# Performance work log

Measured on AMD Instinct MI355X. Metric: run time of the kernel, lower is better.

The kernel has to match this reference:

```python
import jax, jax.numpy as jnp
import numpy as np
import math

N_NODES = 100000
N_EDGES = 3200000
NFEAT = 512
NHID = 256
NCLASS = 16
NLAYERS = 8
LAMDA = 0.5
ALPHA = 0.1


def setup_inputs() -> dict:
    key = jax.random.key(0)
    ks = jax.random.split(key, 10)
    x = jax.random.normal(ks[0], (N_NODES, NFEAT), dtype=jnp.float32)
    edge_src = jax.random.randint(ks[1], (N_EDGES,), 0, N_NODES, dtype=jnp.int32)
    edge_dst = jax.random.randint(ks[2], (N_EDGES,), 0, N_NODES, dtype=jnp.int32)
    edge_w = jax.random.uniform(ks[3], (N_EDGES,), dtype=jnp.float32)
    # fcs[0]: Linear(nfeat, nhidden); fcs[1]: Linear(nhidden, nclass)
    s0 = 1.0 / math.sqrt(NFEAT)
    w0 = jax.random.uniform(ks[4], (NFEAT, NHID), minval=-s0, maxval=s0, dtype=jnp.float32)
    b0 = jax.random.uniform(ks[5], (NHID,), minval=-s0, maxval=s0, dtype=jnp.float32)
    # conv weights: uniform(-1/sqrt(out_features), +), out_features = nhidden
    sc = 1.0 / math.sqrt(NHID)
    conv_w = jax.random.uniform(ks[6], (NLAYERS, NHID, NHID), minval=-sc, maxval=sc, dtype=jnp.float32)
    w1 = jax.random.uniform(ks[7], (NHID, NCLASS), minval=-sc, maxval=sc, dtype=jnp.float32)
    b1 = jax.random.uniform(ks[8], (NCLASS,), minval=-sc, maxval=sc, dtype=jnp.float32)
    return {"x": x, "edge_src": edge_src, "edge_dst": edge_dst, "edge_w": edge_w,
            "w0": w0, "b0": b0, "conv_w": conv_w, "w1": w1, "b1": b1}


def _spmm(edge_src, edge_dst, edge_w, h):
    # torch.spmm(adj, h): out[i] = sum_j adj[i,j] * h[j], adj in COO (dst=row, src=col)
    msgs = edge_w[:, None] * h[edge_src]            # [E, H] irregular gather
    return jax.ops.segment_sum(msgs, edge_dst, num_segments=h.shape[0])


def reference(x, edge_src, edge_dst, edge_w, w0, b0, conv_w, w1, b1):
    # eval mode: F.dropout is identity
    h = jax.nn.relu(x @ w0 + b0)                    # [N, NHID]
    h0 = h
    for i in range(NLAYERS):
        theta = math.log(LAMDA / (i + 1) + 1.0)
        hi = _spmm(edge_src, edge_dst, edge_w, h)   # sparse aggregate
        support = (1.0 - ALPHA) * hi + ALPHA * h0   # initial residual (GCNII)
        out = theta * (support @ conv_w[i]) + (1.0 - theta) * support
        h = jax.nn.relu(out + h)                    # layer residual
    return jax.nn.sigmoid(h @ w1 + b1)              # [N, NCLASS]
```

## Files before the change

kernel.cpp:

```cpp
#include <hip/hip_runtime.h>
#include <math.h>

#define N_NODES 100000
#define N_EDGES 3200000
#define NFEAT 512
#define NHID 256
#define NCLASS 16
#define NLAYERS 8

#define SCAN_CHUNK 1024
#define NB ((N_NODES + SCAN_CHUNK - 1) / SCAN_CHUNK)

typedef float f32x4 __attribute__((ext_vector_type(4)));
typedef short s16x8 __attribute__((ext_vector_type(8)));

__device__ __forceinline__ unsigned short bf16_rne(float f) {
  unsigned u = __float_as_uint(f);
  unsigned r = 0x7fffu + ((u >> 16) & 1u);
  return (unsigned short)((u + r) >> 16);
}
__device__ __forceinline__ float bf16_tof(unsigned short h) {
  return __uint_as_float(((unsigned)h) << 16);
}

__global__ void k_hist(const int* __restrict__ dst, int* __restrict__ cnt) {
  int i = blockIdx.x * 256 + threadIdx.x;
  if (i < N_EDGES) atomicAdd(&cnt[dst[i]], 1);
}

__global__ void k_blocksum(const int* __restrict__ cnt, int* __restrict__ bs) {
  __shared__ int red[256];
  int b = blockIdx.x, t = threadIdx.x;
  int s = 0;
  int base = b * SCAN_CHUNK;
  for (int j = 0; j < 4; ++j) {
    int i = base + t + j * 256;
    if (i < N_NODES) s += cnt[i];
  }
  red[t] = s;
  __syncthreads();
  for (int off = 128; off > 0; off >>= 1) {
    if (t < off) red[t] += red[t + off];
    __syncthreads();
  }
  if (t == 0) bs[b] = red[0];
}

__global__ void k_scan_top(int* __restrict__ bs, int* __restrict__ rp) {
  if (threadIdx.x == 0) {
    int run = 0;
    for (int b = 0; b < NB; ++b) { int v = bs[b]; bs[b] = run; run += v; }
    rp[N_NODES] = run;
  }
}

__global__ void k_scan_write(const int* __restrict__ cnt, const int* __restrict__ bs,
                             int* __restrict__ rp) {
  __shared__ int tot[256];
  int b = blockIdx.x, t = threadIdx.x;
  int base = b * SCAN_CHUNK + t * 4;
  int v0 = 0, v1 = 0, v2 = 0, v3 = 0;
  if (base + 0 < N_NODES) v0 = cnt[base + 0];
  if (base + 1 < N_NODES) v1 = cnt[base + 1];
  if (base + 2 < N_NODES) v2 = cnt[base + 2];
  if (base + 3 < N_NODES) v3 = cnt[base + 3];
  int tsum = v0 + v1 + v2 + v3;
  tot[t] = tsum;
  __syncthreads();
  for (int off = 1; off < 256; off <<= 1) {
    int v = 0;
    if (t >= off) v = tot[t - off];
    __syncthreads();
    if (t >= off) tot[t] += v;
    __syncthreads();
  }
  int excl = tot[t] - tsum + bs[b];
  if (base + 0 < N_NODES) rp[base + 0] = excl;
  if (base + 1 < N_NODES) rp[base + 1] = excl + v0;
  if (base + 2 < N_NODES) rp[base + 2] = excl + v0 + v1;
  if (base + 3 < N_NODES) rp[base + 3] = excl + v0 + v1 + v2;
}

__global__ void k_fill(const int* __restrict__ src, const int* __restrict__ dst,
                       const float* __restrict__ w, const int* __restrict__ rp,
                       int* __restrict__ fill, int* __restrict__ col,
                       float* __restrict__ val) {
  int i = blockIdx.x * 256 + threadIdx.x;
  if (i < N_EDGES) {
    int d = dst[i];
    int pos = rp[d] + atomicAdd(&fill[d], 1);
    col[pos] = src[i];
    val[pos] = w[i];
  }
}

__global__ __launch_bounds__(256)
void k_spmm_half(const int* __restrict__ rp, const int* __restrict__ col,
                 const float* __restrict__ val, const float* __restrict__ h,
                 const float* __restrict__ h0, float* __restrict__ sup, int f0) {
  int wave = threadIdx.x >> 6;
  int lane = threadIdx.x & 63;
  int node = blockIdx.x * 4 + wave;
  if (node >= N_NODES) return;
  int e0 = rp[node], e1 = rp[node + 1];
  const float2* __restrict__ hv = (const float2*)h;
  int fo = (f0 >> 1) + lane;

  float2 a0 = make_float2(0.f, 0.f);
  float2 a1 = make_float2(0.f, 0.f);
  float2 a2 = make_float2(0.f, 0.f);
  float2 a3 = make_float2(0.f, 0.f);

  int e = e0;
  for (; e + 4 <= e1; e += 4) {
    int s0 = col[e], s1 = col[e + 1], s2 = col[e + 2], s3 = col[e + 3];
    float w0 = val[e], w1 = val[e + 1], w2 = val[e + 2], w3 = val[e + 3];
    float2 v0 = hv[(size_t)s0 * 128 + fo];
    float2 v1 = hv[(size_t)s1 * 128 + fo];
    float2 v2 = hv[(size_t)s2 * 128 + fo];
    float2 v3 = hv[(size_t)s3 * 128 + fo];
    a0.x += w0 * v0.x; a0.y += w0 * v0.y;
    a1.x += w1 * v1.x; a1.y += w1 * v1.y;
    a2.x += w2 * v2.x; a2.y += w2 * v2.y;
    a3.x += w3 * v3.x; a3.y += w3 * v3.y;
  }
  for (; e < e1; ++e) {
    int s0 = col[e];
    float w0 = val[e];
    float2 v0 = hv[(size_t)s0 * 128 + fo];
    a0.x += w0 * v0.x; a0.y += w0 * v0.y;
  }

  float2 acc;
  acc.x = (a0.x + a1.x) + (a2.x + a3.x);
  acc.y = (a0.y + a1.y) + (a2.y + a3.y);

  float2 z = ((const float2*)h0)[(size_t)node * 128 + fo];
  float2 o;
  o.x = 0.9f * acc.x + 0.1f * z.x;
  o.y = 0.9f * acc.y + 0.1f * z.y;
  ((float2*)sup)[(size_t)node * 128 + fo] = o;
}

__global__ void k_splitw(const float* __restrict__ W, unsigned short* __restrict__ hi,
                         unsigned short* __restrict__ lo, int K) {
  int mat = blockIdx.y;
  const float* Wm = W + (size_t)mat * K * NHID;
  unsigned short* hm = hi + (size_t)mat * K * NHID;
  unsigned short* lm = lo + (size_t)mat * K * NHID;
  int idx = blockIdx.x * 256 + threadIdx.x;
  if (idx >= K * NHID) return;
  int k = idx >> 8;
  int n = idx & 255;
  float f = Wm[idx];
  unsigned short h = bf16_rne(f);
  unsigned short l = bf16_rne(f - bf16_tof(h));
  hm[(size_t)n * K + k] = h;
  lm[(size_t)n * K + k] = l;
}

#define PADK 40

template <int MODE>
__global__ __launch_bounds__(256)
void k_gemm_mfma(const float* __restrict__ A, const unsigned short* __restrict__ Bh_g,
                 const unsigned short* __restrict__ Bl_g, int K,
                 const float* __restrict__ bias, const float* __restrict__ hin,
                 float* __restrict__ out1, float* __restrict__ out2, float theta) {
  __shared__ unsigned short Ah[128][PADK];
  __shared__ unsigned short Al[128][PADK];
  __shared__ unsigned short Bh[128][PADK];
  __shared__ unsigned short Bl[128][PADK];
  const int bm = blockIdx.x * 128, bn = blockIdx.y * 128;
  const int tid = threadIdx.x;
  const int lane = tid & 63, wave = tid >> 6;
  const int wr = (wave >> 1) * 64;
  const int wc = (wave & 1) * 64;
  const int l16 = lane & 15, lk = lane >> 4;

  f32x4 acc[4][4];
#pragma unroll
  for (int i = 0; i < 4; ++i)
#pragma unroll
    for (int j = 0; j < 4; ++j)
#pragma unroll
      for (int q = 0; q < 4; ++q) acc[i][j][q] = 0.f;

  const int srow = tid >> 3;
  const int skq = (tid & 7) * 4;

  for (int kc = 0; kc < K; kc += 32) {
#pragma unroll
    for (int it = 0; it < 4; ++it) {
      int row = srow + it * 32;
      int gm = bm + row;
      float4 f = make_float4(0.f, 0.f, 0.f, 0.f);
      if (gm < N_NODES) f = *(const float4*)&A[(size_t)gm * K + kc + skq];
      unsigned short h0 = bf16_rne(f.x), h1 = bf16_rne(f.y);
      unsigned short h2 = bf16_rne(f.z), h3 = bf16_rne(f.w);
      ushort4 hv = make_ushort4(h0, h1, h2, h3);
      ushort4 lv = make_ushort4(bf16_rne(f.x - bf16_tof(h0)),
                                bf16_rne(f.y - bf16_tof(h1)),
                                bf16_rne(f.z - bf16_tof(h2)),
                                bf16_rne(f.w - bf16_tof(h3)));
      *(ushort4*)&Ah[row][skq] = hv;
      *(ushort4*)&Al[row][skq] = lv;
    }
#pragma unroll
    for (int it = 0; it < 4; ++it) {
      int row = srow + it * 32;
      size_t go = (size_t)(bn + row) * K + kc + skq;
      *(ushort4*)&Bh[row][skq] = *(const ushort4*)&Bh_g[go];
      *(ushort4*)&Bl[row][skq] = *(const ushort4*)&Bl_g[go];
    }
    __syncthreads();

    s16x8 ah[4], al[4], bh[4], bl[4];
#pragma unroll
    for (int i = 0; i < 4; ++i) {
      ah[i] = *(const s16x8*)&Ah[wr + i * 16 + l16][lk * 8];
      al[i] = *(const s16x8*)&Al[wr + i * 16 + l16][lk * 8];
      bh[i] = *(const s16x8*)&Bh[wc + i * 16 + l16][lk * 8];
      bl[i] = *(const s16x8*)&Bl[wc + i * 16 + l16][lk * 8];
    }
#pragma unroll
    for (int i = 0; i < 4; ++i)
#pragma unroll
      for (int j = 0; j < 4; ++j)
        acc[i][j] = __builtin_amdgcn_mfma_f32_16x16x32_bf16(ah[i], bh[j], acc[i][j], 0, 0, 0);
#pragma unroll
    for (int i = 0; i < 4; ++i)
#pragma unroll
      for (int j = 0; j < 4; ++j)
        acc[i][j] = __builtin_amdgcn_mfma_f32_16x16x32_bf16(ah[i], bl[j], acc[i][j], 0, 0, 0);
#pragma unroll
    for (int i = 0; i < 4; ++i)
#pragma unroll
      for (int j = 0; j < 4; ++j)
        acc[i][j] = __builtin_amdgcn_mfma_f32_16x16x32_bf16(al[i], bh[j], acc[i][j], 0, 0, 0);
    __syncthreads();
  }

  const float omt = 1.f - theta;
#pragma unroll
  for (int i = 0; i < 4; ++i) {
#pragma unroll
    for (int j = 0; j < 4; ++j) {
      int gn = bn + wc + j * 16 + l16;
#pragma unroll
      for (int q = 0; q < 4; ++q) {
        int gm = bm + wr + i * 16 + lk * 4 + q;
        if (gm >= N_NODES) continue;
        size_t r = (size_t)gm * NHID + gn;
        float v = acc[i][j][q];
        if (MODE == 0) {
          float o = fmaxf(v + bias[gn], 0.f);
          out1[r] = o;
          out2[r] = o;
        } else {
          float s = A[r];
          float o = fmaxf(theta * v + omt * s + hin[r], 0.f);
          out1[r] = o;
        }
      }
    }
  }
}

__global__ __launch_bounds__(256)
void k_final(const float* __restrict__ h, const float* __restrict__ w1,
             const float* __restrict__ b1, float* __restrict__ out) {
  __shared__ float ws[NHID * NCLASS];
  int t = threadIdx.x;
  for (int i = t; i < NHID * NCLASS; i += 256) ws[i] = w1[i];
  __syncthreads();
  int node = blockIdx.x * 16 + (t >> 4);
  int c = t & 15;
  if (node >= N_NODES) return;
  float acc = b1[c];
  const float* hr = &h[(size_t)node * NHID];
  for (int k = 0; k < NHID; k += 4) {
    float4 hv = *(const float4*)&hr[k];
    acc += hv.x * ws[(k + 0) * NCLASS + c];
    acc += hv.y * ws[(k + 1) * NCLASS + c];
    acc += hv.z * ws[(k + 2) * NCLASS + c];
    acc += hv.w * ws[(k + 3) * NCLASS + c];
  }
  out[(size_t)node * NCLASS + c] = 1.f / (1.f + __expf(-acc));
}

extern "C" void kernel_launch(void* const* d_in, const int* in_sizes, int n_in,
                              void* d_out, int out_size, void* d_ws, size_t ws_size,
                              hipStream_t stream) {
  const float* x        = (const float*)d_in[0];
  const int*   edge_src = (const int*)d_in[1];
  const int*   edge_dst = (const int*)d_in[2];
  const float* edge_w   = (const float*)d_in[3];
  const float* w0       = (const float*)d_in[4];
  const float* b0       = (const float*)d_in[5];
  const float* conv_w   = (const float*)d_in[6];
  const float* w1       = (const float*)d_in[7];
  const float* b1       = (const float*)d_in[8];
  float* out = (float*)d_out;

  char* ws = (char*)d_ws;
  size_t off = 0;
  auto alloc = [&](size_t bytes) {
    size_t o = off;
    off = (off + bytes + 255) & ~(size_t)255;
    return (void*)(ws + o);
  };
  float* h   = (float*)alloc((size_t)N_NODES * NHID * 4);
  float* h0  = (float*)alloc((size_t)N_NODES * NHID * 4);
  float* sup = (float*)alloc((size_t)N_NODES * NHID * 4);
  int*   rp  = (int*)alloc((size_t)(N_NODES + 1) * 4);
  int*   cnt = (int*)alloc((size_t)N_NODES * 4);
  int*   col = (int*)alloc((size_t)N_EDGES * 4);
  float* val = (float*)alloc((size_t)N_EDGES * 4);
  int*   bs  = (int*)alloc((size_t)NB * 4);
  unsigned short* w0t_hi = (unsigned short*)alloc((size_t)NFEAT * NHID * 2);
  unsigned short* w0t_lo = (unsigned short*)alloc((size_t)NFEAT * NHID * 2);
  unsigned short* cwt_hi = (unsigned short*)alloc((size_t)NLAYERS * NHID * NHID * 2);
  unsigned short* cwt_lo = (unsigned short*)alloc((size_t)NLAYERS * NHID * NHID * 2);
  (void)ws_size;

  (void)hipMemsetAsync(cnt, 0, (size_t)N_NODES * 4, stream);
  k_hist<<<(N_EDGES + 255) / 256, 256, 0, stream>>>(edge_dst, cnt);
  k_blocksum<<<NB, 256, 0, stream>>>(cnt, bs);
  k_scan_top<<<1, 64, 0, stream>>>(bs, rp);
  k_scan_write<<<NB, 256, 0, stream>>>(cnt, bs, rp);
  (void)hipMemsetAsync(cnt, 0, (size_t)N_NODES * 4, stream);
  k_fill<<<(N_EDGES + 255) / 256, 256, 0, stream>>>(edge_src, edge_dst, edge_w, rp,
                                                    cnt, col, val);

  k_splitw<<<dim3((NFEAT * NHID + 255) / 256, 1), 256, 0, stream>>>(w0, w0t_hi, w0t_lo, NFEAT);
  k_splitw<<<dim3((NHID * NHID + 255) / 256, NLAYERS), 256, 0, stream>>>(conv_w, cwt_hi, cwt_lo, NHID);

  dim3 g0((N_NODES + 127) / 128, NHID / 128);
  k_gemm_mfma<0><<<g0, 256, 0, stream>>>(x, w0t_hi, w0t_lo, NFEAT, b0, nullptr, h, h0, 0.f);

  for (int i = 0; i < NLAYERS; ++i) {
    float theta = logf(0.5f / (float)(i + 1) + 1.0f);
    k_spmm_half<<<(N_NODES + 3) / 4, 256, 0, stream>>>(rp, col, val, h, h0, sup, 0);
    k_spmm_half<<<(N_NODES + 3) / 4, 256, 0, stream>>>(rp, col, val, h, h0, sup, 128);
    const unsigned short* whi = cwt_hi + (size_t)i * NHID * NHID;
    const unsigned short* wlo = cwt_lo + (size_t)i * NHID * NHID;
    k_gemm_mfma<1><<<g0, 256, 0, stream>>>(sup, whi, wlo, NHID, nullptr, h, h, nullptr, theta);
  }

  k_final<<<(N_NODES + 15) / 16, 256, 0, stream>>>(h, w1, b1, out);
}
```

Measured before the change: 5.855 ms.

## Pre-split SpMM output to bf16 hi/lo and double-buffer full-width MFMA GEMM

The SpMM now writes its support output already split into bf16 hi/lo halves, so the layer GEMM no longer converts fp32 A tiles itself. The GEMM becomes a 512-thread kernel covering all 256 output columns per block, so A is read once instead of once per column half. It streams A and B into double-buffered LDS via async global-to-LDS loads, overlapping loads with MFMA. The epilogue stages results through LDS for coalesced float4 stores. This adds a large LDS footprint (96KB) that limits occupancy, and the residual term is rebuilt from the hi+lo pair instead of read as fp32.

```diff
diff --git a/kernel.cpp b/kernel.cpp
--- a/kernel.cpp
+++ b/kernel.cpp
@@ -21,6 +21,12 @@
 }
 __device__ __forceinline__ float bf16_tof(unsigned short h) {
   return __uint_as_float(((unsigned)h) << 16);
+}
+
+__device__ __forceinline__ void async16(void* lds_dst, const void* gsrc) {
+  __builtin_amdgcn_global_load_lds(
+      (const __attribute__((address_space(1))) unsigned int*)gsrc,
+      (__attribute__((address_space(3))) unsigned int*)lds_dst, 16, 0, 0);
 }
 
 __global__ void k_hist(const int* __restrict__ dst, int* __restrict__ cnt) {
@@ -97,7 +103,9 @@
 __global__ __launch_bounds__(256)
 void k_spmm_half(const int* __restrict__ rp, const int* __restrict__ col,
                  const float* __restrict__ val, const float* __restrict__ h,
-                 const float* __restrict__ h0, float* __restrict__ sup, int f0) {
+                 const float* __restrict__ h0,
+                 unsigned short* __restrict__ sup_hi,
+                 unsigned short* __restrict__ sup_lo, int f0) {
   int wave = threadIdx.x >> 6;
   int lane = threadIdx.x & 63;
   int node = blockIdx.x * 4 + wave;
@@ -136,10 +144,13 @@
   acc.y = (a0.y + a1.y) + (a2.y + a3.y);
 
   float2 z = ((const float2*)h0)[(size_t)node * 128 + fo];
-  float2 o;
-  o.x = 0.9f * acc.x + 0.1f * z.x;
-  o.y = 0.9f * acc.y + 0.1f * z.y;
-  ((float2*)sup)[(size_t)node * 128 + fo] = o;
+  float ox = 0.9f * acc.x + 0.1f * z.x;
+  float oy = 0.9f * acc.y + 0.1f * z.y;
+  unsigned short hx = bf16_rne(ox), hy = bf16_rne(oy);
+  unsigned short lx = bf16_rne(ox - bf16_tof(hx));
+  unsigned short ly = bf16_rne(oy - bf16_tof(hy));
+  ((ushort2*)sup_hi)[(size_t)node * 128 + fo] = make_ushort2(hx, hy);
+  ((ushort2*)sup_lo)[(size_t)node * 128 + fo] = make_ushort2(lx, ly);
 }
 
 __global__ void k_splitw(const float* __restrict__ W, unsigned short* __restrict__ hi,
@@ -159,24 +170,21 @@
   lm[(size_t)n * K + k] = l;
 }
 
-#define PADK 40
-
 template <int MODE>
-__global__ __launch_bounds__(256)
-void k_gemm_mfma(const float* __restrict__ A, const unsigned short* __restrict__ Bh_g,
-                 const unsigned short* __restrict__ Bl_g, int K,
-                 const float* __restrict__ bias, const float* __restrict__ hin,
-                 float* __restrict__ out1, float* __restrict__ out2, float theta) {
-  __shared__ unsigned short Ah[128][PADK];
-  __shared__ unsigned short Al[128][PADK];
-  __shared__ unsigned short Bh[128][PADK];
-  __shared__ unsigned short Bl[128][PADK];
-  const int bm = blockIdx.x * 128, bn = blockIdx.y * 128;
+__global__ __launch_bounds__(512)
+void k_gemm2(const float* __restrict__ Af,
+             const unsigned short* __restrict__ Ah_g,
+             const unsigned short* __restrict__ Al_g,
+             const unsigned short* __restrict__ Bh_g,
+             const unsigned short* __restrict__ Bl_g, int K,
+             const float* __restrict__ bias, const float* __restrict__ hin,
+             float* __restrict__ out1, float* __restrict__ out2, float theta) {
+  __shared__ unsigned short pool[49152];
   const int tid = threadIdx.x;
-  const int lane = tid & 63, wave = tid >> 6;
-  const int wr = (wave >> 1) * 64;
-  const int wc = (wave & 1) * 64;
+  const int lane = tid & 63, w = tid >> 6;
+  const int wr = w >> 2, wc = w & 3;
   const int l16 = lane & 15, lk = lane >> 4;
+  const int bm = blockIdx.x * 128;
 
   f32x4 acc[4][4];
 #pragma unroll
@@ -186,42 +194,74 @@
 #pragma unroll
       for (int q = 0; q < 4; ++q) acc[i][j][q] = 0.f;
 
-  const int srow = tid >> 3;
-  const int skq = (tid & 7) * 4;
-
-  for (int kc = 0; kc < K; kc += 32) {
-#pragma unroll
-    for (int it = 0; it < 4; ++it) {
-      int row = srow + it * 32;
-      int gm = bm + row;
-      float4 f = make_float4(0.f, 0.f, 0.f, 0.f);
-      if (gm < N_NODES) f = *(const float4*)&A[(size_t)gm * K + kc + skq];
-      unsigned short h0 = bf16_rne(f.x), h1 = bf16_rne(f.y);
-      unsigned short h2 = bf16_rne(f.z), h3 = bf16_rne(f.w);
+  auto stageB = [&](int buf, int kc) {
+#pragma unroll
+    for (int u = 0; u < 2; ++u) {
+      int fb = w * 2 + u;
+      size_t go = (size_t)(fb * 16 + l16) * K + kc + lk * 8;
+      async16(&pool[16384 + buf * 8192 + fb * 512], &Bh_g[go]);
+      async16(&pool[32768 + buf * 8192 + fb * 512], &Bl_g[go]);
+    }
+  };
+  auto stageA1 = [&](int buf, int kc) {
+    size_t go = (size_t)(bm + w * 16 + l16) * K + kc + lk * 8;
+    async16(&pool[0 + buf * 4096 + w * 512], &Ah_g[go]);
+    async16(&pool[8192 + buf * 4096 + w * 512], &Al_g[go]);
+  };
+  float4 fa0, fa1;
+  auto stageA0_issue = [&](int kc) {
+    int m0 = tid >> 3, k00 = (tid & 7) * 4;
+    int m1 = (tid + 512) >> 3, k01 = ((tid + 512) & 7) * 4;
+    fa0 = make_float4(0.f, 0.f, 0.f, 0.f);
+    fa1 = fa0;
+    if (bm + m0 < N_NODES) fa0 = *(const float4*)&Af[(size_t)(bm + m0) * K + kc + k00];
+    if (bm + m1 < N_NODES) fa1 = *(const float4*)&Af[(size_t)(bm + m1) * K + kc + k01];
+  };
+  auto stageA0_write = [&](int buf) {
+#pragma unroll
+    for (int p = 0; p < 2; ++p) {
+      int f = tid + p * 512;
+      int m = f >> 3, k0 = (f & 7) * 4;
+      float4 fv = p ? fa1 : fa0;
+      int L = (m >> 4) * 64 + (m & 15) + (k0 >> 3) * 16;
+      unsigned short h0 = bf16_rne(fv.x), h1 = bf16_rne(fv.y);
+      unsigned short h2 = bf16_rne(fv.z), h3 = bf16_rne(fv.w);
       ushort4 hv = make_ushort4(h0, h1, h2, h3);
-      ushort4 lv = make_ushort4(bf16_rne(f.x - bf16_tof(h0)),
-                                bf16_rne(f.y - bf16_tof(h1)),
-                                bf16_rne(f.z - bf16_tof(h2)),
-                                bf16_rne(f.w - bf16_tof(h3)));
-      *(ushort4*)&Ah[row][skq] = hv;
-      *(ushort4*)&Al[row][skq] = lv;
-    }
-#pragma unroll
-    for (int it = 0; it < 4; ++it) {
-      int row = srow + it * 32;
-      size_t go = (size_t)(bn + row) * K + kc + skq;
-      *(ushort4*)&Bh[row][skq] = *(const ushort4*)&Bh_g[go];
-      *(ushort4*)&Bl[row][skq] = *(const ushort4*)&Bl_g[go];
-    }
-    __syncthreads();
-
+      ushort4 lv = make_ushort4(bf16_rne(fv.x - bf16_tof(h0)),
+                                bf16_rne(fv.y - bf16_tof(h1)),
+                                bf16_rne(fv.z - bf16_tof(h2)),
+                                bf16_rne(fv.w - bf16_tof(h3)));
+      *(ushort4*)&pool[0 + buf * 4096 + L * 8 + (k0 & 7)] = hv;
+      *(ushort4*)&pool[8192 + buf * 4096 + L * 8 + (k0 & 7)] = lv;
+    }
+  };
+
+  if (MODE == 0) { stageA0_issue(0); stageA0_write(0); }
+  else stageA1(0, 0);
+  stageB(0, 0);
+  __syncthreads();
+
+  const int nt = K / 32;
+  int buf = 0;
+  for (int t = 0; t < nt; ++t) {
+    const bool pf = (t + 1 < nt);
+    if (pf) {
+      if (MODE == 0) stageA0_issue((t + 1) * 32);
+      else stageA1(buf ^ 1, (t + 1) * 32);
+      stageB(buf ^ 1, (t + 1) * 32);
+    }
     s16x8 ah[4], al[4], bh[4], bl[4];
 #pragma unroll
     for (int i = 0; i < 4; ++i) {
-      ah[i] = *(const s16x8*)&Ah[wr + i * 16 + l16][lk * 8];
-      al[i] = *(const s16x8*)&Al[wr + i * 16 + l16][lk * 8];
-      bh[i] = *(const s16x8*)&Bh[wc + i * 16 + l16][lk * 8];
-      bl[i] = *(const s16x8*)&Bl[wc + i * 16 + l16][lk * 8];
+      int fb = wr * 4 + i;
+      ah[i] = *(const s16x8*)&pool[0 + buf * 4096 + fb * 512 + lane * 8];
+      al[i] = *(const s16x8*)&pool[8192 + buf * 4096 + fb * 512 + lane * 8];
+    }
+#pragma unroll
+    for (int j = 0; j < 4; ++j) {
+      int fb = wc * 4 + j;
+      bh[j] = *(const s16x8*)&pool[16384 + buf * 8192 + fb * 512 + lane * 8];
+      bl[j] = *(const s16x8*)&pool[32768 + buf * 8192 + fb * 512 + lane * 8];
     }
 #pragma unroll
     for (int i = 0; i < 4; ++i)
@@ -238,32 +278,64 @@
 #pragma unroll
       for (int j = 0; j < 4; ++j)
         acc[i][j] = __builtin_amdgcn_mfma_f32_16x16x32_bf16(al[i], bh[j], acc[i][j], 0, 0, 0);
-    __syncthreads();
-  }
-
+    if (MODE == 0 && pf) stageA0_write(buf ^ 1);
+    __syncthreads();
+    buf ^= 1;
+  }
+
+  float* Cst = (float*)pool;
   const float omt = 1.f - theta;
-#pragma unroll
-  for (int i = 0; i < 4; ++i) {
-#pragma unroll
-    for (int j = 0; j < 4; ++j) {
-      int gn = bn + wc + j * 16 + l16;
-#pragma unroll
-      for (int q = 0; q < 4; ++q) {
-        int gm = bm + wr + i * 16 + lk * 4 + q;
-        if (gm >= N_NODES) continue;
-        size_t r = (size_t)gm * NHID + gn;
-        float v = acc[i][j][q];
-        if (MODE == 0) {
-          float o = fmaxf(v + bias[gn], 0.f);
-          out1[r] = o;
-          out2[r] = o;
-        } else {
-          float s = A[r];
-          float o = fmaxf(theta * v + omt * s + hin[r], 0.f);
-          out1[r] = o;
+  for (int g = 0; g < 4; ++g) {
+    if (wr == (g >> 1)) {
+#pragma unroll
+      for (int ii = 0; ii < 2; ++ii) {
+        int i = (g & 1) * 2 + ii;
+#pragma unroll
+        for (int j = 0; j < 4; ++j) {
+          int colc = wc * 64 + j * 16 + l16;
+#pragma unroll
+          for (int q = 0; q < 4; ++q) {
+            int lr = ii * 16 + lk * 4 + q;
+            Cst[lr * 260 + colc] = acc[i][j][q];
+          }
         }
       }
     }
+    __syncthreads();
+#pragma unroll
+    for (int p = 0; p < 4; ++p) {
+      int f = tid + p * 512;
+      int row = f >> 6, c4 = (f & 63) * 4;
+      int gm = bm + g * 32 + row;
+      if (gm < N_NODES) {
+        float4 v = *(const float4*)&Cst[row * 260 + c4];
+        size_t r = (size_t)gm * NHID + c4;
+        float4 o;
+        if (MODE == 0) {
+          float4 bb = *(const float4*)&bias[c4];
+          o.x = fmaxf(v.x + bb.x, 0.f);
+          o.y = fmaxf(v.y + bb.y, 0.f);
+          o.z = fmaxf(v.z + bb.z, 0.f);
+          o.w = fmaxf(v.w + bb.w, 0.f);
+          *(float4*)&out1[r] = o;
+          *(float4*)&out2[r] = o;
+        } else {
+          ushort4 sh = *(const ushort4*)&Ah_g[r];
+          ushort4 sl = *(const ushort4*)&Al_g[r];
+          float4 hv = *(const float4*)&hin[r];
+          float sx = bf16_tof(sh.x) + bf16_tof(sl.x);
+          float sy = bf16_tof(sh.y) + bf16_tof(sl.y);
+          float sz = bf16_tof(sh.z) + bf16_tof(sl.z);
+          float sw = bf16_tof(sh.w) + bf16_tof(sl.w);
+          o.x = fmaxf(theta * v.x + omt * sx + hv.x, 0.f);
+          o.y = fmaxf(theta * v.y + omt * sy + hv.y, 0.f);
+          o.z = fmaxf(theta * v.z + omt * sz + hv.z, 0.f);
+          o.w = fmaxf(theta * v.w + omt * sw + hv.w, 0.f);
+          *(float4*)&out1[r] = o;
+        }
+      }
+    }
+    __syncthreads();
   }
 }
 
@@ -310,13 +382,14 @@
     off = (off + bytes + 255) & ~(size_t)255;
     return (void*)(ws + o);
   };
-  float* h   = (float*)alloc((size_t)N_NODES * NHID * 4);
-  float* h0  = (float*)alloc((size_t)N_NODES * NHID * 4);
-  float* sup = (float*)alloc((size_t)N_NODES * NHID * 4);
+  float* h    = (float*)alloc((size_t)N_NODES * NHID * 4);
+  float* h0   = (float*)alloc((size_t)N_NODES * NHID * 4);
+  unsigned short* sup_hi = (unsigned short*)alloc((size_t)N_NODES * NHID * 2);
+  unsigned short* sup_lo = (unsigned short*)alloc((size_t)N_NODES * NHID * 2);
+  int*   col = (int*)alloc((size_t)N_EDGES * 4);
+  float* val = (float*)alloc((size_t)N_EDGES * 4);
   int*   rp  = (int*)alloc((size_t)(N_NODES + 1) * 4);
   int*   cnt = (int*)alloc((size_t)N_NODES * 4);
-  int*   col = (int*)alloc((size_t)N_EDGES * 4);
-  float* val = (float*)alloc((size_t)N_EDGES * 4);
   int*   bs  = (int*)alloc((size_t)NB * 4);
   unsigned short* w0t_hi = (unsigned short*)alloc((size_t)NFEAT * NHID * 2);
   unsigned short* w0t_lo = (unsigned short*)alloc((size_t)NFEAT * NHID * 2);
@@ -336,16 +409,20 @@
   k_splitw<<<dim3((NFEAT * NHID + 255) / 256, 1), 256, 0, stream>>>(w0, w0t_hi, w0t_lo, NFEAT);
   k_splitw<<<dim3((NHID * NHID + 255) / 256, NLAYERS), 256, 0, stream>>>(conv_w, cwt_hi, cwt_lo, NHID);
 
-  dim3 g0((N_NODES + 127) / 128, NHID / 128);
-  k_gemm_mfma<0><<<g0, 256, 0, stream>>>(x, w0t_hi, w0t_lo, NFEAT, b0, nullptr, h, h0, 0.f);
+  int gblocks = (N_NODES + 127) / 128;
+  k_gemm2<0><<<gblocks, 512, 0, stream>>>(x, nullptr, nullptr, w0t_hi, w0t_lo,
+                                          NFEAT, b0, nullptr, h, h0, 0.f);
 
   for (int i = 0; i < NLAYERS; ++i) {
     float theta = logf(0.5f / (float)(i + 1) + 1.0f);
-    k_spmm_half<<<(N_NODES + 3) / 4, 256, 0, stream>>>(rp, col, val, h, h0, sup, 0);
-    k_spmm_half<<<(N_NODES + 3) / 4, 256, 0, stream>>>(rp, col, val, h, h0, sup, 128);
+    k_spmm_half<<<(N_NODES + 3) / 4, 256, 0, stream>>>(rp, col, val, h, h0,
+                                                       sup_hi, sup_lo, 0);
+    k_spmm_half<<<(N_NODES + 3) / 4, 256, 0, stream>>>(rp, col, val, h, h0,
+                                                       sup_hi, sup_lo, 128);
     const unsigned short* whi = cwt_hi + (size_t)i * NHID * NHID;
     const unsigned short* wlo = cwt_lo + (size_t)i * NHID * NHID;
-    k_gemm_mfma<1><<<g0, 256, 0, stream>>>(sup, whi, wlo, NHID, nullptr, h, h, nullptr, theta);
+    k_gemm2<1><<<gblocks, 512, 0, stream>>>(nullptr, sup_hi, sup_lo, whi, wlo,
+                                            NHID, nullptr, h, h, nullptr, theta);
   }
 
   k_final<<<(N_NODES + 15) / 16, 256, 0, stream>>>(h, w1, b1, out);
```

Result: faster. 5.297 ms (-9.5%).
